# Kernel tuning notes

Measured on AMD Instinct MI355X. Metric: run time of the kernel, lower is better.

## Reference

```python
import jax, jax.numpy as jnp
import numpy as np

N = 50000
E = 500000
IN_C = 100
HID = 80
OUT = 80
EDGE_DIM = 100
NUM_AGGR = 6
NUM_SCALE = 5

# PNA degree statistics, computed from the degree histogram exactly as PyG does
DEG_HIST = np.array([240, 328, 79, 39, 23, 12, 11, 7, 6, 5, 7, 3, 1, 0, 2, 0, 0, 0, 1], dtype=np.float64)
_bins = np.arange(len(DEG_HIST), dtype=np.float64)
_tot = DEG_HIST.sum()
AVG_LIN = np.float32((_bins * DEG_HIST).sum() / _tot)
AVG_LOG = np.float32((np.log(_bins + 1.0) * DEG_HIST).sum() / _tot)


def _lin_init(key, fan_in, fan_out):
    k1, k2 = jax.random.split(key)
    bound = 1.0 / np.sqrt(fan_in)
    W = jax.random.uniform(k1, (fan_in, fan_out), minval=-bound, maxval=bound, dtype=jnp.float32)
    b = jax.random.uniform(k2, (fan_out,), minval=-bound, maxval=bound, dtype=jnp.float32)
    return W, b


def setup_inputs() -> dict:
    key = jax.random.key(0)
    ks = jax.random.split(key, 20)
    inp = {}
    inp["x1"] = jax.random.normal(ks[0], (N, IN_C), jnp.float32)
    inp["edge_index1"] = jax.random.randint(ks[1], (2, E), 0, N)
    inp["edge_attr1"] = jax.random.normal(ks[2], (E, EDGE_DIM), jnp.float32)
    inp["x2"] = jax.random.normal(ks[3], (N, IN_C), jnp.float32)
    inp["edge_index2"] = jax.random.randint(ks[4], (2, E), 0, N)
    inp["edge_attr2"] = jax.random.normal(ks[5], (E, EDGE_DIM), jnp.float32)
    # conv1 params (F_in=100 -> F_out=80)
    inp["We1"], inp["be1"] = _lin_init(ks[6], EDGE_DIM, IN_C)
    inp["Wpre1"], inp["bpre1"] = _lin_init(ks[7], 3 * IN_C, IN_C)
    inp["Wpost1"], inp["bpost1"] = _lin_init(ks[8], (NUM_AGGR * NUM_SCALE + 1) * IN_C, HID)
    inp["Wlin1"], inp["blin1"] = _lin_init(ks[9], HID, HID)
    # conv2 params (F_in=80 -> F_out=80)
    inp["We2"], inp["be2"] = _lin_init(ks[10], EDGE_DIM, HID)
    inp["Wpre2"], inp["bpre2"] = _lin_init(ks[11], 3 * HID, HID)
    inp["Wpost2"], inp["bpost2"] = _lin_init(ks[12], (NUM_AGGR * NUM_SCALE + 1) * HID, OUT)
    inp["Wlin2"], inp["blin2"] = _lin_init(ks[13], OUT, OUT)
    # MLP head
    inp["Wfc1"], inp["bfc1"] = _lin_init(ks[14], OUT, 80)
    inp["Wfc2"], inp["bfc2"] = _lin_init(ks[15], 80, OUT)
    return inp


def _pna(x, src, dst, edge_attr, We, be, Wpre, bpre, Wpost, bpost, Wlin, blin):
    """PNAConv, towers=1, pre_layers=1, post_layers=1, divide_input=False."""
    F_in = x.shape[1]
    e = edge_attr @ We + be                                    # [E, F] edge encoder
    # pre_nn(cat([x_i, x_j, e])) done as 3 matmuls to avoid [E, 3F] concat
    W_i, W_j, W_e = Wpre[:F_in], Wpre[F_in:2 * F_in], Wpre[2 * F_in:]
    h = x[dst] @ W_i + x[src] @ W_j + e @ W_e + bpre           # [E, F] messages
    cnt = jax.ops.segment_sum(jnp.ones((h.shape[0],), h.dtype), dst, N)  # in-degree
    deg = jnp.maximum(cnt, 1.0)
    s = jax.ops.segment_sum(h, dst, N)                         # sum aggr
    mean = s / deg[:, None]
    mean_sq = jax.ops.segment_sum(h * h, dst, N) / deg[:, None]
    var = mean_sq - mean * mean
    std = jnp.sqrt(jnp.maximum(var, 0.0) + 1e-5)
    has = (cnt > 0)[:, None]
    mn = jnp.where(has, jax.ops.segment_min(h, dst, N), 0.0)
    mx = jnp.where(has, jax.ops.segment_max(h, dst, N), 0.0)
    agg = jnp.concatenate([s, mean, mn, mx, var, std], axis=-1)  # [N, 6F]
    logd = jnp.log(deg + 1.0)
    scaled = jnp.concatenate([
        agg,
        agg * (logd / AVG_LOG)[:, None],     # amplification
        agg * (AVG_LOG / logd)[:, None],     # attenuation
        agg * (deg / AVG_LIN)[:, None],      # linear
        agg * (AVG_LIN / deg)[:, None],      # inverse_linear
    ], axis=-1)                              # [N, 30F]
    out = jnp.concatenate([x, scaled], axis=-1) @ Wpost + bpost  # post_nn
    return out @ Wlin + blin


def _branch(x, edge_index, edge_attr, c1, c2, Wfc1, bfc1, Wfc2, bfc2):
    src, dst = edge_index[0], edge_index[1]
    x = jax.nn.relu(_pna(x, src, dst, edge_attr, *c1))
    x = _pna(x, src, dst, edge_attr, *c2)
    x = jax.nn.relu(x @ Wfc1 + bfc1)
    return x @ Wfc2 + bfc2


def reference(x1, edge_index1, edge_attr1, x2, edge_index2, edge_attr2,
              We1, be1, Wpre1, bpre1, Wpost1, bpost1, Wlin1, blin1,
              We2, be2, Wpre2, bpre2, Wpost2, bpost2, Wlin2, blin2,
              Wfc1, bfc1, Wfc2, bfc2):
    c1 = (We1, be1, Wpre1, bpre1, Wpost1, bpost1, Wlin1, blin1)
    c2 = (We2, be2, Wpre2, bpre2, Wpost2, bpost2, Wlin2, blin2)
    out1 = _branch(x1, edge_index1, edge_attr1, c1, c2, Wfc1, bfc1, Wfc2, bfc2)
    out2 = _branch(x2, edge_index2, edge_attr2, c1, c2, Wfc1, bfc1, Wfc2, bfc2)
    return (out1, out2)
```

## Files before the change

kernel.cpp:

```cpp
#include <hip/hip_runtime.h>
#include <cmath>

static constexpr int NN = 50000;
static constexpr int EE = 500000;

typedef short v8s __attribute__((ext_vector_type(8)));
typedef float v4f __attribute__((ext_vector_type(4)));

__device__ inline short f2bf(float x){
  union{float f; unsigned u;} v{x};
  unsigned r = v.u + 0x7fffu + ((v.u >> 16) & 1u);
  return (short)(r >> 16);
}
__device__ inline float b2f(short s){
  union{unsigned u; float f;} v; v.u = ((unsigned)(unsigned short)s) << 16; return v.f;
}
__device__ inline unsigned cvtpk(float lo, float hi){
  unsigned r;
  asm("v_cvt_pk_bf16_f32 %0, %1, %2" : "=v"(r) : "v"(lo), "v"(hi));
  return r;
}
__device__ inline void gload16(const void* gp, void* lp){
  __builtin_amdgcn_global_load_lds(
      (const __attribute__((address_space(1))) void*)gp,
      (__attribute__((address_space(3))) void*)lp,
      16, 0, 0);
}


__global__ __launch_bounds__(256)
void count_deg_k(const int* __restrict__ dst, int* __restrict__ cnt, int e_total){
  int e = blockIdx.x*256 + threadIdx.x;
  if (e < e_total) atomicAdd(&cnt[dst[e]], 1);
}

__global__ __launch_bounds__(1024)
void scan_block_k(const int* __restrict__ cnt, int* __restrict__ pre,
                  int* __restrict__ bsum, int n){
  __shared__ int tmp[1024];
  int b = blockIdx.x, t = threadIdx.x, i = b*1024 + t;
  int v = (i < n) ? cnt[i] : 0;
  tmp[t] = v; __syncthreads();
  for (int off = 1; off < 1024; off <<= 1){
    int u = (t >= off) ? tmp[t-off] : 0;
    __syncthreads();
    tmp[t] += u;
    __syncthreads();
  }
  if (i < n) pre[i] = tmp[t];
  if (t == 1023) bsum[b] = tmp[t];
}

__global__ void scan_sums_k(int* __restrict__ bsum, int nb){
  if (threadIdx.x == 0){
    int s = 0;
    for (int i = 0; i < nb; i++){ int v = bsum[i]; bsum[i] = s; s += v; }
  }
}

__global__ __launch_bounds__(256)
void scan_finalize_k(const int* __restrict__ pre, const int* __restrict__ bsum,
                     int* __restrict__ offs, int n){
  int i = blockIdx.x*256 + threadIdx.x;
  if (i < n) offs[i+1] = pre[i] + bsum[i >> 10];
  if (i == 0) offs[0] = 0;
}

__global__ __launch_bounds__(256)
void fill_csr_k(const int* __restrict__ dst, const int* __restrict__ src,
                const int* __restrict__ offs, int* __restrict__ cursor,
                int* __restrict__ srcs_csr, int* __restrict__ pos, int e_total){
  int e = blockIdx.x*256 + threadIdx.x;
  if (e < e_total){
    int d = dst[e];
    int p = offs[d] + atomicAdd(&cursor[d], 1);
    srcs_csr[p] = src[e];
    pos[e] = p;
  }
}


struct VJob { const float* v; const float* B; const float* b2; float* out; int K, Nc; };
struct VJobs { VJob j[3]; };
__global__ __launch_bounds__(128)
void vecmat_multi_k(VJobs js){
  const VJob J = js.j[blockIdx.y];
  int c = threadIdx.x;
  if (c < J.Nc){
    float s = J.b2[c];
    for (int k = 0; k < J.K; k++) s += J.v[k]*J.B[(size_t)k*J.Nc + c];
    J.out[c] = s;
  }
}

__global__ __launch_bounds__(256)
void sgemm_k(const float* __restrict__ A, const float* __restrict__ B,
             float* __restrict__ C, int M, int K, int Nc){
  __shared__ float As[16][65];
  __shared__ float Bs[16][65];
  int bm = blockIdx.x*64, bn = blockIdx.y*64;
  int tid = threadIdx.x;
  int tx = tid & 15, ty = tid >> 4;
  float acc[4][4] = {};
  for (int k0 = 0; k0 < K; k0 += 16){
    #pragma unroll
    for (int i = 0; i < 4; i++){
      int t = tid + 256*i;
      int r = t >> 4, c = t & 15;
      int gr = bm + r, gc = k0 + c;
      As[c][r] = (gr < M && gc < K) ? A[(size_t)gr*K + gc] : 0.f;
    }
    #pragma unroll
    for (int i = 0; i < 4; i++){
      int t = tid + 256*i;
      int r = t >> 6, c = t & 63;
      int gr = k0 + r, gc = bn + c;
      Bs[r][c] = (gr < K && gc < Nc) ? B[(size_t)gr*Nc + gc] : 0.f;
    }
    __syncthreads();
    #pragma unroll
    for (int kk = 0; kk < 16; kk++){
      float a[4], b[4];
      #pragma unroll
      for (int i = 0; i < 4; i++) a[i] = As[kk][ty*4 + i];
      #pragma unroll
      for (int j = 0; j < 4; j++) b[j] = Bs[kk][tx*4 + j];
      #pragma unroll
      for (int i = 0; i < 4; i++)
        #pragma unroll
        for (int j = 0; j < 4; j++) acc[i][j] += a[i]*b[j];
    }
    __syncthreads();
  }
  #pragma unroll
  for (int i = 0; i < 4; i++){
    int gr = bm + ty*4 + i;
    if (gr >= M) continue;
    #pragma unroll
    for (int j = 0; j < 4; j++){
      int gc = bn + tx*4 + j;
      if (gc < Nc) C[(size_t)gr*Nc + gc] = acc[i][j];
    }
  }
}

struct TJob { const float* src; short* dst; int K, ldsrc, Ncols; };
struct TJobs { TJob j[9]; };
__global__ __launch_bounds__(128)
void tconv_multi_k(TJobs js){
  const TJob J = js.j[blockIdx.y];
  int c = blockIdx.x;
  int k = threadIdx.x;
  if (c < J.Ncols)
    J.dst[(long)c*128 + k] = (k < J.K) ? f2bf(J.src[(long)k*J.ldsrc + c]) : (short)0;
}

__global__ __launch_bounds__(256)
void btpost_k(const float* __restrict__ Wpost, int F, int Kpad,
              short* __restrict__ dst){
  int cp = blockIdx.x;
  int k = blockIdx.y*256 + threadIdx.x;
  if (k >= Kpad) return;
  int g = cp / 80, c = cp - g*80;
  float v = 0.f;
  if (k < F){ if (g == 0) v = Wpost[(long)k*80 + c]; }
  else if (k < 7*F) v = Wpost[(long)(F + g*6*F + (k - F))*80 + c];
  dst[(long)cp*Kpad + k] = f2bf(v);
}

__global__ __launch_bounds__(256)
void cvt_rows_k(const float* __restrict__ src, int K, short* __restrict__ dst,
                int ldd, long total){
  long i = (long)blockIdx.x*256 + threadIdx.x;
  if (i >= total) return;
  int n = (int)(i / K), c = (int)(i - (long)n*K);
  dst[(long)n*ldd + c] = f2bf(src[i]);
}

struct ZJob { short* p; int ld, c0, nc, rows; };
struct ZJobs { ZJob j[4]; };
__global__ __launch_bounds__(256)
void zeropad_k(ZJobs js){
  const ZJob J = js.j[blockIdx.y];
  int i = blockIdx.x*256 + threadIdx.x;
  int r = i / J.nc, c = i - r*J.nc;
  if (r < J.rows) J.p[(long)r*J.ld + J.c0 + c] = 0;
}

__global__ __launch_bounds__(256)
void epgemm_k(const float* __restrict__ ea,
              const short* __restrict__ Bt,
              const float* __restrict__ bias,
              const int* __restrict__ pos,
              short* __restrict__ epc)
{
  __shared__ float Atile[3456];
  __shared__ short stage[32*200];
  int tid = threadIdx.x, w = tid >> 6, lane = tid & 63;
  int lr = lane & 15, lkg = lane >> 4;

  v8s bfrag[3][4];
  float bvs[3];
  #pragma unroll
  for (int n = 0; n < 3; n++){
    int col = w*48 + n*16 + lr;
    bvs[n] = bias[col];
    #pragma unroll
    for (int ks = 0; ks < 4; ks++)
      bfrag[n][ks] = *(const v8s*)(Bt + (long)col*128 + ks*32 + lkg*8);
  }

  const char* srcbase = (const char*)ea;
  const char* srcend  = srcbase + (long)EE*400 - 16;
  const int Mtiles = EE/32;

  for (int t = blockIdx.x; t < Mtiles; t += gridDim.x){
    long tb = (long)t*12800;
    for (int c = w; c < 13; c += 4){
      const char* src = srcbase + tb + (long)c*1024 + lane*16;
      if (src > srcend) src = srcend;
      gload16(src, (char*)Atile + c*1024);
    }
    __syncthreads();

    const float* rp0 = Atile + lr*100;
    const float* rp1 = Atile + (16 + lr)*100;
    v8s a0[4], a1[4];
    #pragma unroll
    for (int ks = 0; ks < 4; ks++){
      float4 lo0, hi0, lo1, hi1;
      if (ks < 3){
        int kb = ks*32 + lkg*8;
        lo0 = *(const float4*)(rp0 + kb); hi0 = *(const float4*)(rp0 + kb + 4);
        lo1 = *(const float4*)(rp1 + kb); hi1 = *(const float4*)(rp1 + kb + 4);
      } else {
        float4 z = make_float4(0.f,0.f,0.f,0.f);
        lo0 = (lkg == 0) ? *(const float4*)(rp0 + 96) : z;
        lo1 = (lkg == 0) ? *(const float4*)(rp1 + 96) : z;
        hi0 = z; hi1 = z;
      }
      union { v8s s; unsigned u[4]; } o0, o1;
      o0.u[0] = cvtpk(lo0.x, lo0.y); o0.u[1] = cvtpk(lo0.z, lo0.w);
      o0.u[2] = cvtpk(hi0.x, hi0.y); o0.u[3] = cvtpk(hi0.z, hi0.w);
      o1.u[0] = cvtpk(lo1.x, lo1.y); o1.u[1] = cvtpk(lo1.z, lo1.w);
      o1.u[2] = cvtpk(hi1.x, hi1.y); o1.u[3] = cvtpk(hi1.z, hi1.w);
      a0[ks] = o0.s; a1[ks] = o1.s;
    }
    v4f acc0[3], acc1[3];
    #pragma unroll
    for (int n = 0; n < 3; n++){ acc0[n] = (v4f)0.f; acc1[n] = (v4f)0.f; }
    #pragma unroll
    for (int ks = 0; ks < 4; ks++){
      #pragma unroll
      for (int n = 0; n < 3; n++){
        acc0[n] = __builtin_amdgcn_mfma_f32_16x16x32_bf16(a0[ks], bfrag[n][ks], acc0[n], 0, 0, 0);
        acc1[n] = __builtin_amdgcn_mfma_f32_16x16x32_bf16(a1[ks], bfrag[n][ks], acc1[n], 0, 0, 0);
      }
    }

    #pragma unroll
    for (int n = 0; n < 3; n++){
      int col = w*48 + n*16 + lr;
      #pragma unroll
      for (int j = 0; j < 4; j++){
        stage[(lkg*4 + j)*200 + col]      = f2bf(acc0[n][j] + bvs[n]);
        stage[(16 + lkg*4 + j)*200 + col] = f2bf(acc1[n][j] + bvs[n]);
      }
    }
    __syncthreads();

    #pragma unroll
    for (int i = 0; i < 3; i++){
      int u = i*256 + tid;
      int r = u / 24, ch = u - r*24;
      int prow = pos[t*32 + r];
      *(v8s*)(epc + (long)prow*192 + ch*8) = *(const v8s*)&stage[r*200 + ch*8];
    }
  }
}

template<int NFR, bool C_F32, bool RELU>
__global__ __launch_bounds__(256)
void egemm_k(const short* __restrict__ Ab, long lda,
             const short* __restrict__ Bt, const float* __restrict__ bias,
             void* __restrict__ Cv, long ldc, int M, int ncols, int wlim)
{
  constexpr int BN = NFR*16;
  constexpr int PITCH = BN + 8;
  constexpr int NCH = 2*NFR;
  __shared__ short Bs[BN][136];
  __shared__ short stage[4*8*PITCH];
  short* Cb = (short*)Cv;
  float* Cf = (float*)Cv;

  int bn = blockIdx.y*BN;
  for (int u = threadIdx.x; u < BN*16; u += 256){
    int c = u >> 4, k8 = (u & 15)*8;
    v8s vv = (v8s)0;
    if (bn + c < ncols) vv = *(const v8s*)(Bt + (long)(bn + c)*128 + k8);
    *(v8s*)&Bs[c][k8] = vv;
  }
  __syncthreads();

  int lane = threadIdx.x & 63;
  int lr = lane & 15, lkg = lane >> 4;
  int w = threadIdx.x >> 6;
  short* st = stage + w*8*PITCH;
  int w0 = (blockIdx.x*256 + threadIdx.x) >> 6;
  int nw = gridDim.x * 4;
  int Mtiles = (M + 31) >> 5;

  float bvs[NFR];
  #pragma unroll
  for (int n = 0; n < NFR; n++) bvs[n] = bias ? bias[bn + n*16 + lr] : 0.f;

  for (int t = w0; t < Mtiles; t += nw){
    int base = t*32;
    long r0 = base + lr;      if (r0 > M-1) r0 = M-1;
    long r1 = base + 16 + lr; if (r1 > M-1) r1 = M-1;

    v8s a0[4], a1[4];
    const short* p0 = Ab + r0*lda + lkg*8;
    const short* p1 = Ab + r1*lda + lkg*8;
    #pragma unroll
    for (int ks = 0; ks < 4; ks++){
      a0[ks] = *(const v8s*)(p0 + ks*32);
      a1[ks] = *(const v8s*)(p1 + ks*32);
    }

    v4f acc0[NFR], acc1[NFR];
    #pragma unroll
    for (int n = 0; n < NFR; n++){ acc0[n] = (v4f)0.f; acc1[n] = (v4f)0.f; }
    #pragma unroll
    for (int ks = 0; ks < 4; ks++){
      #pragma unroll
      for (int n = 0; n < NFR; n++){
        v8s b = *(const v8s*)&Bs[n*16 + lr][ks*32 + lkg*8];
        acc0[n] = __builtin_amdgcn_mfma_f32_16x16x32_bf16(a0[ks], b, acc0[n], 0, 0, 0);
        acc1[n] = __builtin_amdgcn_mfma_f32_16x16x32_bf16(a1[ks], b, acc1[n], 0, 0, 0);
      }
    }

    if constexpr (C_F32){
      #pragma unroll
      for (int n = 0; n < NFR; n++){
        int col = bn + n*16 + lr;
        if (col >= ncols) continue;
        #pragma unroll
        for (int j = 0; j < 4; j++){
          int row = base + lkg*4 + j;
          float v0 = acc0[n][j] + bvs[n];
          float v1 = acc1[n][j] + bvs[n];
          if (RELU){ v0 = fmaxf(v0, 0.f); v1 = fmaxf(v1, 0.f); }
          if (row < M)      Cf[(long)row*ldc + col] = v0;
          if (row + 16 < M) Cf[(long)(row+16)*ldc + col] = v1;
        }
      }
    } else {
      #pragma unroll
      for (int q = 0; q < 4; q++){
        if ((lkg >> 1) == (q & 1)){
          int srow = (lkg & 1)*4;
          #pragma unroll
          for (int n = 0; n < NFR; n++){
            #pragma unroll
            for (int j = 0; j < 4; j++){
              float v = ((q < 2) ? acc0[n][j] : acc1[n][j]) + bvs[n];
              if (RELU) v = fmaxf(v, 0.f);
              st[(srow + j)*PITCH + n*16 + lr] = f2bf(v);
            }
          }
        }
        int rb = base + q*8;
        #pragma unroll
        for (int i = 0; i < (8*NCH + 63)/64; i++){
          int c = i*64 + lane;
          if (c < 8*NCH){
            int r = c/NCH, off8 = (c - r*NCH)*8;
            int grow = rb + r;
            if (grow < M && bn + off8 < wlim)
              *(v8s*)(Cb + (long)grow*ldc + bn + off8) = *(const v8s*)&st[r*PITCH + off8];
          }
        }
      }
    }
  }
}

__global__ __launch_bounds__(512)
void pgemm_k(const short* __restrict__ Ab, int kpad,
             const short* __restrict__ Bt, const float* __restrict__ scl,
             const float* __restrict__ bias, short* __restrict__ C, int M)
{
  __shared__ short Bs[400][40];
  __shared__ short AsSt[10240];
  short (*As)[40] = (short(*)[40])AsSt;

  int tid = threadIdx.x;
  int w = tid >> 6, lane = tid & 63;
  int lr = lane & 15, lkg = lane >> 4;
  int bm = blockIdx.x*128;

  v4f acc[25];
  #pragma unroll
  for (int n = 0; n < 25; n++) acc[n] = (v4f)0.f;

  for (int k0 = 0; k0 < kpad; k0 += 32){
    {
      int u = tid;
      int r = u >> 2, c8 = (u & 3)*8;
      int grow = bm + r;
      v8s out = (v8s)0;
      if (grow < M) out = *(const v8s*)(Ab + (long)grow*kpad + k0 + c8);
      *(v8s*)&As[r][c8] = out;
    }
    for (int u = tid; u < 400*4; u += 512){
      int c = u >> 2, k8 = (u & 3)*8;
      *(v8s*)&Bs[c][k8] = *(const v8s*)(Bt + (long)c*kpad + k0 + k8);
    }
    __syncthreads();
    {
      v8s a = *(const v8s*)&As[w*16 + lr][lkg*8];
      #pragma unroll
      for (int n = 0; n < 25; n++){
        v8s b = *(const v8s*)&Bs[n*16 + lr][lkg*8];
        acc[n] = __builtin_amdgcn_mfma_f32_16x16x32_bf16(a, b, acc[n], 0, 0, 0);
      }
    }
    __syncthreads();
  }

  short* st = AsSt + w*16*80;
  float sc[4][5];
  #pragma unroll
  for (int j = 0; j < 4; j++){
    int row = bm + w*16 + lkg*4 + j;
    int rr = row < M ? row : 0;
    #pragma unroll
    for (int g = 0; g < 5; g++) sc[j][g] = scl[rr*5 + g];
  }
  #pragma unroll
  for (int cc = 0; cc < 5; cc++){
    float bv = bias[cc*16 + lr];
    #pragma unroll
    for (int j = 0; j < 4; j++){
      float v = bv;
      #pragma unroll
      for (int g = 0; g < 5; g++) v += sc[j][g]*acc[5*g + cc][j];
      st[(lkg*4 + j)*80 + cc*16 + lr] = f2bf(v);
    }
  }
  #pragma unroll
  for (int i = 0; i < 3; i++){
    int c = i*64 + lane;
    if (c < 160){
      int r = c/10, off = (c - r*10)*8;
      int grow = bm + w*16 + r;
      if (grow < M)
        *(v8s*)(C + (long)grow*128 + off) = *(const v8s*)&st[r*80 + off];
    }
  }
}

template<int F>
__global__ __launch_bounds__(256)
void aggregate_k(const short* __restrict__ xixj, int ldx,
                 const short* __restrict__ epc, int epoff,
                 const int* __restrict__ srcs_csr,
                 const int* __restrict__ offs,
                 short* __restrict__ aggout, long ldk,
                 float* __restrict__ scl, float avg_lin, float avg_log, int n){
  int wnode = (blockIdx.x*256 + threadIdx.x) >> 6;
  int lane = threadIdx.x & 63;
  if (wnode >= n) return;
  constexpr int C2 = F - 64;
  int beg = offs[wnode], end = offs[wnode+1];
  float xi0 = b2f(xixj[(long)wnode*ldx + lane]);
  float xi1 = (lane < C2) ? b2f(xixj[(long)wnode*ldx + 64 + lane]) : 0.f;
  float s0 = 0.f, q0 = 0.f, mn0 = INFINITY, mx0 = -INFINITY;
  float s1 = 0.f, q1 = 0.f, mn1 = INFINITY, mx1 = -INFINITY;
  for (int p = beg; p < end; p++){
    int s = srcs_csr[p];
    float h0 = xi0 + b2f(xixj[(long)s*ldx + F + lane]) + b2f(epc[(long)p*192 + epoff + lane]);
    s0 += h0; q0 += h0*h0; mn0 = fminf(mn0, h0); mx0 = fmaxf(mx0, h0);
    if (lane < C2){
      float h1 = xi1 + b2f(xixj[(long)s*ldx + F + 64 + lane]) + b2f(epc[(long)p*192 + epoff + 64 + lane]);
      s1 += h1; q1 += h1*h1; mn1 = fminf(mn1, h1); mx1 = fmaxf(mx1, h1);
    }
  }
  int cnt = end - beg;
  float deg = (float)(cnt > 1 ? cnt : 1);
  if (cnt == 0){ mn0 = 0.f; mx0 = 0.f; mn1 = 0.f; mx1 = 0.f; }
  float mean0 = s0/deg, var0 = q0/deg - mean0*mean0;
  float std0 = sqrtf(fmaxf(var0, 0.f) + 1e-5f);
  short* a = aggout + (long)wnode*ldk;
  a[lane] = f2bf(s0); a[F+lane] = f2bf(mean0); a[2*F+lane] = f2bf(mn0);
  a[3*F+lane] = f2bf(mx0); a[4*F+lane] = f2bf(var0); a[5*F+lane] = f2bf(std0);
  if (lane < C2){
    float mean1 = s1/deg, var1 = q1/deg - mean1*mean1;
    float std1 = sqrtf(fmaxf(var1, 0.f) + 1e-5f);
    int l2 = 64 + lane;
    a[l2] = f2bf(s1); a[F+l2] = f2bf(mean1); a[2*F+l2] = f2bf(mn1);
    a[3*F+l2] = f2bf(mx1); a[4*F+l2] = f2bf(var1); a[5*F+l2] = f2bf(std1);
  }
  if (lane == 0){
    float logd = logf(deg + 1.f);
    scl[wnode*5+0] = 1.f;
    scl[wnode*5+1] = logd/avg_log;
    scl[wnode*5+2] = avg_log/logd;
    scl[wnode*5+3] = deg/avg_lin;
    scl[wnode*5+4] = avg_lin/deg;
  }
}


extern "C" void kernel_launch(void* const* d_in, const int* in_sizes, int n_in,
                              void* d_out, int out_size, void* d_ws, size_t ws_size,
                              hipStream_t stream){
  const float* x1   = (const float*)d_in[0];
  const int*   ei1  = (const int*)  d_in[1];
  const float* ea1  = (const float*)d_in[2];
  const float* x2   = (const float*)d_in[3];
  const int*   ei2  = (const int*)  d_in[4];
  const float* ea2  = (const float*)d_in[5];
  const float* We1  = (const float*)d_in[6],  *be1   = (const float*)d_in[7];
  const float* Wpre1= (const float*)d_in[8],  *bpre1 = (const float*)d_in[9];
  const float* Wpost1=(const float*)d_in[10], *bpost1= (const float*)d_in[11];
  const float* Wlin1= (const float*)d_in[12], *blin1 = (const float*)d_in[13];
  const float* We2  = (const float*)d_in[14], *be2   = (const float*)d_in[15];
  const float* Wpre2= (const float*)d_in[16], *bpre2 = (const float*)d_in[17];
  const float* Wpost2=(const float*)d_in[18], *bpost2= (const float*)d_in[19];
  const float* Wlin2= (const float*)d_in[20], *blin2 = (const float*)d_in[21];
  const float* Wfc1 = (const float*)d_in[22], *bfc1  = (const float*)d_in[23];
  const float* Wfc2 = (const float*)d_in[24], *bfc2  = (const float*)d_in[25];

  static const double HIST[19] = {240,328,79,39,23,12,11,7,6,5,7,3,1,0,2,0,0,0,1};
  double tot = 0, lin = 0, lg = 0;
  for (int i = 0; i < 19; i++){ tot += HIST[i]; lin += i*HIST[i]; lg += log((double)i + 1.0)*HIST[i]; }
  float avg_lin = (float)(lin/tot), avg_log = (float)(lg/tot);

  const int KP1 = 704, KP2 = 576;

  uintptr_t pw = (uintptr_t)d_ws;
  auto carve = [&](size_t b)->void*{ void* r = (void*)pw; pw += (b + 255) & ~(size_t)255; return r; };
  int*   cnt      = (int*)  carve((size_t)NN*4);
  int*   cursor   = (int*)  carve((size_t)NN*4);
  int*   pre      = (int*)  carve((size_t)NN*4);
  int*   bsum     = (int*)  carve(64*4);
  int*   offs     = (int*)  carve((size_t)(NN+1)*4);
  int*   srcs_csr = (int*)  carve((size_t)EE*4);
  int*   pos      = (int*)  carve((size_t)EE*4);
  float* WecA     = (float*)carve(100*100*4);
  float* WecB     = (float*)carve(100*80*4);
  float* Wlf      = (float*)carve(80*80*4);
  float* becf     = (float*)carve(256*4);
  float* blf      = (float*)carve(128*4);
  short* Btep12   = (short*)carve((size_t)192*128*2);
  short* Btij1    = (short*)carve((size_t)208*128*2);
  short* Btij2    = (short*)carve((size_t)160*128*2);
  short* Btpost1  = (short*)carve((size_t)400*KP1*2);
  short* Btpost2  = (short*)carve((size_t)400*KP2*2);
  short* Btlin1   = (short*)carve((size_t)80*128*2);
  short* Btlf     = (short*)carve((size_t)80*128*2);
  short* Btfc2    = (short*)carve((size_t)80*128*2);
  short* Aprime1  = (short*)carve((size_t)NN*KP1*2);
  short* Aprime2  = (short*)carve((size_t)NN*KP2*2);
  short* xixjb    = (short*)carve((size_t)NN*224*2);
  short* epc      = (short*)carve((size_t)EE*192*2);
  float* scl      = (float*)carve((size_t)NN*5*4);
  short* tpost    = (short*)carve((size_t)NN*128*2);
  short* tD       = (short*)carve((size_t)NN*128*2);

  dim3 blk(256);
  const int NB = (NN + 1023)/1024;
  const int GB_N = 391;

  sgemm_k<<<dim3(2,2), blk, 0, stream>>>(We1, Wpre1 + 2*100*100, WecA, 100, 100, 100);
  sgemm_k<<<dim3(2,2), blk, 0, stream>>>(We2, Wpre2 + 2*80*80,  WecB, 100, 80, 80);
  sgemm_k<<<dim3(2,2), blk, 0, stream>>>(Wlin2, Wfc1, Wlf, 80, 80, 80);
  hipMemsetAsync(becf, 0, 256*4, stream);
  {
    VJobs vj;
    vj.j[0] = {be1,  Wpre1 + 2*100*100, bpre1, becf,       100, 100};
    vj.j[1] = {be2,  Wpre2 + 2*80*80,   bpre2, becf + 100,  80,  80};
    vj.j[2] = {blin2, Wfc1,             bfc1,  blf,         80,  80};
    vecmat_multi_k<<<dim3(1,3), dim3(128), 0, stream>>>(vj);
  }
  {
    TJobs tj;
    tj.j[0] = {WecA,            Btep12,            100, 100, 100};
    tj.j[1] = {WecB,            Btep12 + 100*128,  100,  80,  80};
    tj.j[2] = {Wpre1,           Btij1,             100, 100, 100};
    tj.j[3] = {Wpre1 + 100*100, Btij1 + 100*128,   100, 100, 100};
    tj.j[4] = {Wpre2,           Btij2,              80,  80,  80};
    tj.j[5] = {Wpre2 + 80*80,   Btij2 + 80*128,     80,  80,  80};
    tj.j[6] = {Wlin1,           Btlin1,             80,  80,  80};
    tj.j[7] = {Wlf,             Btlf,               80,  80,  80};
    tj.j[8] = {Wfc2,            Btfc2,              80,  80,  80};
    tconv_multi_k<<<dim3(100,9), dim3(128), 0, stream>>>(tj);
  }
  hipMemsetAsync(Btep12 + 180*128, 0, (size_t)12*128*2, stream);
  hipMemsetAsync(Btij1 + 200*128, 0, (size_t)8*128*2, stream);
  btpost_k<<<dim3(400,(KP1+255)/256), blk, 0, stream>>>(Wpost1, 100, KP1, Btpost1);
  btpost_k<<<dim3(400,(KP2+255)/256), blk, 0, stream>>>(Wpost2,  80, KP2, Btpost2);
  {
    ZJobs zj;
    zj.j[0] = {Aprime1, KP1, 700,  4, NN};
    zj.j[1] = {Aprime2, KP2, 560, 16, NN};
    zj.j[2] = {tpost,   128,  80, 48, NN};
    zj.j[3] = {tD,      128,  80, 48, NN};
    zeropad_k<<<dim3((NN*48 + 255)/256, 4), blk, 0, stream>>>(zj);
  }

  for (int b = 0; b < 2; b++){
    const float* x  = b ? x2  : x1;
    const int*   ei = b ? ei2 : ei1;
    const float* ea = b ? ea2 : ea1;
    float* outb = (float*)d_out + (size_t)b*NN*80;
    const int* src = ei;
    const int* dst = ei + EE;

    hipMemsetAsync(cnt, 0, (uintptr_t)pre - (uintptr_t)cnt, stream);
    count_deg_k<<<dim3((EE+255)/256), blk, 0, stream>>>(dst, cnt, EE);
    scan_block_k<<<dim3(NB), dim3(1024), 0, stream>>>(cnt, pre, bsum, NN);
    scan_sums_k<<<dim3(1), dim3(64), 0, stream>>>(bsum, NB);
    scan_finalize_k<<<dim3((NN+255)/256), blk, 0, stream>>>(pre, bsum, offs, NN);
    fill_csr_k<<<dim3((EE+255)/256), blk, 0, stream>>>(dst, src, offs, cursor, srcs_csr, pos, EE);

    epgemm_k<<<dim3(2048), blk, 0, stream>>>(ea, Btep12, becf, pos, epc);

    cvt_rows_k<<<dim3((int)(((long)NN*100 + 255)/256)), blk, 0, stream>>>(x, 100, Aprime1, KP1, (long)NN*100);

    egemm_k<5,false,false><<<dim3(GB_N,3), blk, 0, stream>>>(
        Aprime1, KP1, Btij1, nullptr, xixjb, 224, NN, 200, 200);
    aggregate_k<100><<<dim3((NN+3)/4), blk, 0, stream>>>(
        xixjb, 224, epc, 0, srcs_csr, offs, Aprime1 + 100, KP1, scl, avg_lin, avg_log, NN);
    pgemm_k<<<dim3((NN+127)/128), dim3(512), 0, stream>>>(
        Aprime1, KP1, Btpost1, scl, bpost1, tpost, NN);
    egemm_k<5,false,true><<<dim3(GB_N,1), blk, 0, stream>>>(
        tpost, 128, Btlin1, blin1, Aprime2, KP2, NN, 80, 80);

    egemm_k<5,false,false><<<dim3(GB_N,2), blk, 0, stream>>>(
        Aprime2, KP2, Btij2, nullptr, xixjb, 160, NN, 160, 160);
    aggregate_k<80><<<dim3((NN+3)/4), blk, 0, stream>>>(
        xixjb, 160, epc, 100, srcs_csr, offs, Aprime2 + 80, KP2, scl, avg_lin, avg_log, NN);
    pgemm_k<<<dim3((NN+127)/128), dim3(512), 0, stream>>>(
        Aprime2, KP2, Btpost2, scl, bpost2, tpost, NN);

    egemm_k<5,false,true><<<dim3(GB_N,1), blk, 0, stream>>>(
        tpost, 128, Btlf, blf, tD, 128, NN, 80, 80);
    egemm_k<5,true,false><<<dim3(GB_N,1), blk, 0, stream>>>(
        tD, 128, Btfc2, bfc2, outb, 80, NN, 80, 80);
  }
}
```

Measured before the change: 1.222 ms.

## Double-buffer edge-attribute tile loads in edge projection GEMM

Splits the LDS tile for edge attributes in epgemm_k into two buffers and prefetches the next tile with global-to-LDS loads while the current tile is converted, multiplied and scattered. It replaces full __syncthreads with explicit vmcnt/lgkmcnt waits sized to each wave's number of outstanding loads, plus raw barriers. The aim is to hide global memory latency on the large edge_attr stream. In exchange it uses more LDS, which may lower occupancy, and it relies on hand-tuned waitcnt values that must match the load counts per wave.

```diff
diff --git a/kernel.cpp b/kernel.cpp
--- a/kernel.cpp
+++ b/kernel.cpp
@@ -194,7 +194,7 @@
               const int* __restrict__ pos,
               short* __restrict__ epc)
 {
-  __shared__ float Atile[3456];
+  __shared__ float Atile[2][3328];
   __shared__ short stage[32*200];
   int tid = threadIdx.x, w = tid >> 6, lane = tid & 63;
   int lr = lane & 15, lkg = lane >> 4;
@@ -213,18 +213,40 @@
   const char* srcbase = (const char*)ea;
   const char* srcend  = srcbase + (long)EE*400 - 16;
   const int Mtiles = EE/32;
-
-  for (int t = blockIdx.x; t < Mtiles; t += gridDim.x){
-    long tb = (long)t*12800;
+  const int stride = gridDim.x;
+
+  int t0 = blockIdx.x;
+  if (t0 >= Mtiles) return;
+
+  {
+    long tb = (long)t0*12800;
     for (int c = w; c < 13; c += 4){
       const char* src = srcbase + tb + (long)c*1024 + lane*16;
       if (src > srcend) src = srcend;
-      gload16(src, (char*)Atile + c*1024);
-    }
-    __syncthreads();
-
-    const float* rp0 = Atile + lr*100;
-    const float* rp1 = Atile + (16 + lr)*100;
+      gload16(src, (char*)&Atile[0][0] + c*1024);
+    }
+  }
+
+  int cur = 0;
+  for (int t = t0; t < Mtiles; t += stride){
+    int tn = t + stride;
+    if (tn < Mtiles){
+      long tb = (long)tn*12800;
+      for (int c = w; c < 13; c += 4){
+        const char* src = srcbase + tb + (long)c*1024 + lane*16;
+        if (src > srcend) src = srcend;
+        gload16(src, (char*)&Atile[cur^1][0] + c*1024);
+      }
+      if (w == 0) asm volatile("s_waitcnt vmcnt(4)" ::: "memory");
+      else        asm volatile("s_waitcnt vmcnt(3)" ::: "memory");
+    } else {
+      asm volatile("s_waitcnt vmcnt(0)" ::: "memory");
+    }
+    __builtin_amdgcn_sched_barrier(0);
+    __builtin_amdgcn_s_barrier();
+
+    const float* rp0 = &Atile[cur][0] + lr*100;
+    const float* rp1 = &Atile[cur][0] + (16 + lr)*100;
     v8s a0[4], a1[4];
     #pragma unroll
     for (int ks = 0; ks < 4; ks++){
@@ -267,7 +289,9 @@
         stage[(16 + lkg*4 + j)*200 + col] = f2bf(acc1[n][j] + bvs[n]);
       }
     }
-    __syncthreads();
+    asm volatile("s_waitcnt lgkmcnt(0)" ::: "memory");
+    __builtin_amdgcn_sched_barrier(0);
+    __builtin_amdgcn_s_barrier();
 
     #pragma unroll
     for (int i = 0; i < 3; i++){
@@ -276,6 +300,7 @@
       int prow = pos[t*32 + r];
       *(v8s*)(epc + (long)prow*192 + ch*8) = *(const v8s*)&stage[r*200 + ch*8];
     }
+    cur ^= 1;
   }
 }
 
```

Measured after the change: 1.218 ms. Within noise of the previous version (-0.3%).
